# Kernel tuning notes

Hardware: AMD Instinct MI355X
Metric: run time of the kernel (lower is better)

## Reference

```python
import jax, jax.numpy as jnp
import numpy as np

M, Q, H, L = 1, 9, 512, 2

def lstm_seq(x, w_ih, w_hh, b, reverse=False):
    # x: [B, T, Din] -> outputs [B, T, H], final (h, c) each [B, H]
    B = x.shape[0]
    h0 = jnp.zeros((B, H), x.dtype)
    xw = jnp.einsum('btd,gd->btg', x, w_ih) + b  # [B, T, 4H] input projection, precomputed
    def step(carry, xt):
        h, c = carry
        g = xt + h @ w_hh.T
        i, f, gg, o = jnp.split(g, 4, axis=-1)  # torch gate order: i, f, g, o
        c = jax.nn.sigmoid(f) * c + jax.nn.sigmoid(i) * jnp.tanh(gg)
        h = jax.nn.sigmoid(o) * jnp.tanh(c)
        return (h, c), h
    (hT, cT), hs = jax.lax.scan(step, (h0, h0), jnp.swapaxes(xw, 0, 1), reverse=reverse)
    return jnp.swapaxes(hs, 0, 1), hT, cT

def _forward(X, future_features, Y_teacher,
             enc_w_ih_l0, enc_w_hh_l0, enc_b_l0, enc_w_ih_l0r, enc_w_hh_l0r, enc_b_l0r,
             enc_w_ih_l1, enc_w_hh_l1, enc_b_l1, enc_w_ih_l1r, enc_w_hh_l1r, enc_b_l1r,
             dec_w_ih_l0, dec_w_hh_l0, dec_b_l0, dec_w_ih_l1, dec_w_hh_l1, dec_b_l1,
             bidi_w_h, bidi_b_h, out_w, out_b, horizon_span):
    B = X.shape[0]
    enc = [((enc_w_ih_l0, enc_w_hh_l0, enc_b_l0), (enc_w_ih_l0r, enc_w_hh_l0r, enc_b_l0r)),
           ((enc_w_ih_l1, enc_w_hh_l1, enc_b_l1), (enc_w_ih_l1r, enc_w_hh_l1r, enc_b_l1r))]
    inp, hs, cs = X, [], []
    for fw, bw in enc:  # bidirectional multilayer encoder
        of, hf, cf = lstm_seq(inp, *fw, reverse=False)
        ob, hb, cb = lstm_seq(inp, *bw, reverse=True)
        inp = jnp.concatenate([of, ob], axis=-1)
        hs += [hf, hb]; cs += [cf, cb]
    h = jnp.stack(hs)  # [2L, B, H], torch order (l0_fwd, l0_bwd, l1_fwd, l1_bwd)
    c = jnp.stack(cs)
    def merge(s):  # NOTE: original applies bidi_project__h / nonlin__h to BOTH h and c
        s = s.reshape(L, 2, B, H)
        s = jnp.concatenate([s[:, 0], s[:, 1]], axis=2)       # [L, B, 2H]
        s = jnp.swapaxes(s, 0, 1).reshape(B, 2 * L * H)
        s = jax.nn.elu(s @ bidi_w_h.T + bidi_b_h)             # [B, L*H]
        return jnp.swapaxes(s.reshape(B, L, H), 0, 1)         # [L, B, H]
    h, c = merge(h), merge(c)
    dec = [(dec_w_ih_l0, dec_w_hh_l0, dec_b_l0), (dec_w_ih_l1, dec_w_hh_l1, dec_b_l1)]
    def dec_step(carry, f_t):
        h, c, y_prev = carry
        x = jnp.concatenate([y_prev, f_t], axis=-1)  # [B, M + d_future_features]
        nh, nc = [], []
        for l, (w_ih, w_hh, b) in enumerate(dec):
            g = x @ w_ih.T + h[l] @ w_hh.T + b
            i, f, gg, o = jnp.split(g, 4, axis=-1)
            cl = jax.nn.sigmoid(f) * c[l] + jax.nn.sigmoid(i) * jnp.tanh(gg)
            x = jax.nn.sigmoid(o) * jnp.tanh(cl)
            nh.append(x); nc.append(cl)
        y = x @ out_w.T + out_b                       # [B, M*Q]
        return (jnp.stack(nh), jnp.stack(nc), y[:, :M]), y
    y0 = X[:, -1, :M]
    _, ys = jax.lax.scan(dec_step, (h, c, y0), jnp.swapaxes(future_features, 0, 1))
    T = future_features.shape[1]
    return jnp.swapaxes(ys, 0, 1).reshape(B, T, M, Q)

def setup_inputs() -> dict:
    key = jax.random.key(0)
    ks = iter(jax.random.split(key, 40))
    s = 0.05
    d = {
        'X': jax.random.normal(next(ks), (64, 256, 9), jnp.float32),
        'future_features': jax.random.normal(next(ks), (64, 96, 8), jnp.float32),
        'Y_teacher': jax.random.normal(next(ks), (64, 96, 1), jnp.float32),
    }
    shapes = {
        'enc_w_ih_l0': (2048, 9), 'enc_w_hh_l0': (2048, 512), 'enc_b_l0': (2048,),
        'enc_w_ih_l0r': (2048, 9), 'enc_w_hh_l0r': (2048, 512), 'enc_b_l0r': (2048,),
        'enc_w_ih_l1': (2048, 1024), 'enc_w_hh_l1': (2048, 512), 'enc_b_l1': (2048,),
        'enc_w_ih_l1r': (2048, 1024), 'enc_w_hh_l1r': (2048, 512), 'enc_b_l1r': (2048,),
        'dec_w_ih_l0': (2048, 9), 'dec_w_hh_l0': (2048, 512), 'dec_b_l0': (2048,),
        'dec_w_ih_l1': (2048, 512), 'dec_w_hh_l1': (2048, 512), 'dec_b_l1': (2048,),
        'bidi_w_h': (1024, 2048), 'bidi_b_h': (1024,),
        'out_w': (9, 512), 'out_b': (9,),
    }
    for name, shp in shapes.items():
        d[name] = jax.random.normal(next(ks), shp, jnp.float32) * s
    d['horizon_span'] = 96
    return d

def reference(X, future_features, Y_teacher,
              enc_w_ih_l0, enc_w_hh_l0, enc_b_l0, enc_w_ih_l0r, enc_w_hh_l0r, enc_b_l0r,
              enc_w_ih_l1, enc_w_hh_l1, enc_b_l1, enc_w_ih_l1r, enc_w_hh_l1r, enc_b_l1r,
              dec_w_ih_l0, dec_w_hh_l0, dec_b_l0, dec_w_ih_l1, dec_w_hh_l1, dec_b_l1,
              bidi_w_h, bidi_b_h, out_w, out_b, horizon_span):
    return _forward(X, future_features, Y_teacher,
                    enc_w_ih_l0, enc_w_hh_l0, enc_b_l0, enc_w_ih_l0r, enc_w_hh_l0r, enc_b_l0r,
                    enc_w_ih_l1, enc_w_hh_l1, enc_b_l1, enc_w_ih_l1r, enc_w_hh_l1r, enc_b_l1r,
                    dec_w_ih_l0, dec_w_hh_l0, dec_b_l0, dec_w_ih_l1, dec_w_hh_l1, dec_b_l1,
                    bidi_w_h, bidi_b_h, out_w, out_b, horizon_span)
```

## Files before the change

### kernel.cpp

```cpp
#include <hip/hip_runtime.h>


#define BLOCKS 256

typedef short bf16x8 __attribute__((ext_vector_type(8)));
typedef float f32x4  __attribute__((ext_vector_type(4)));
typedef unsigned short u16;

__device__ __forceinline__ f32x4 MFMA16(bf16x8 a, bf16x8 b, f32x4 c) {
  return __builtin_amdgcn_mfma_f32_16x16x32_bf16(a, b, c, 0, 0, 0);
}

__device__ __forceinline__ u16 bfr(float f) {
  unsigned u = __float_as_uint(f);
  u += 0x7FFFu + ((u >> 16) & 1u);
  return (u16)(u >> 16);
}
__device__ __forceinline__ bf16x8 pack8(float4 a, float4 b) {
  bf16x8 r;
  r[0] = (short)bfr(a.x); r[1] = (short)bfr(a.y); r[2] = (short)bfr(a.z); r[3] = (short)bfr(a.w);
  r[4] = (short)bfr(b.x); r[5] = (short)bfr(b.y); r[6] = (short)bfr(b.z); r[7] = (short)bfr(b.w);
  return r;
}
__device__ __forceinline__ bf16x8 loadW8(const float* p) {
  float4 a = *(const float4*)p;
  float4 b = *(const float4*)(p + 4);
  return pack8(a, b);
}
__device__ __forceinline__ float sigm(float x) { return 1.0f / (1.0f + __expf(-x)); }
__device__ __forceinline__ float tanh_f(float x) {
  float a = fabsf(x);
  float e = __expf(-2.0f * a);
  float t = (1.0f - e) / (1.0f + e);
  return x < 0.0f ? -t : t;
}
__device__ __forceinline__ float lstm_h(const float pre[4], float& c) {
  float ig = sigm(pre[0]);
  float fg = sigm(pre[1]);
  float gg = tanh_f(pre[2]);
  float og = sigm(pre[3]);
  c = fg * c + ig * gg;
  return og * tanh_f(c);
}

__device__ __forceinline__ void st_b16_coh(u16* p, u16 v) {
  unsigned uv = v;
  asm volatile("global_store_short %0, %1, off sc0 sc1" :: "v"(p), "v"(uv) : "memory");
}
__device__ __forceinline__ void st_f32_coh(float* p, float v) {
  asm volatile("global_store_dword %0, %1, off sc0 sc1" :: "v"(p), "v"(v) : "memory");
}
__device__ __forceinline__ void st_u32_coh(unsigned* p, unsigned v) {
  asm volatile("global_store_dword %0, %1, off sc0 sc1" :: "v"(p), "v"(v) : "memory");
}
__device__ __forceinline__ float ld_f32_coh(const float* p) {
  float r;
  asm volatile("global_load_dword %0, %1, off sc0 sc1\n\ts_waitcnt vmcnt(0)"
               : "=&v"(r) : "v"(p) : "memory");
  return r;
}
__device__ __forceinline__ unsigned ld_u32_coh(const unsigned* p) {
  unsigned r;
  asm volatile("global_load_dword %0, %1, off sc0 sc1\n\ts_waitcnt vmcnt(0)"
               : "=&v"(r) : "v"(p) : "memory");
  return r;
}
__device__ __forceinline__ void ld_tile_coh(const u16* base, bf16x8 f[16]) {
  asm volatile(
    "global_load_dwordx4 %0, %16, off sc0 sc1\n\t"
    "global_load_dwordx4 %1, %16, off offset:64 sc0 sc1\n\t"
    "global_load_dwordx4 %2, %16, off offset:128 sc0 sc1\n\t"
    "global_load_dwordx4 %3, %16, off offset:192 sc0 sc1\n\t"
    "global_load_dwordx4 %4, %16, off offset:256 sc0 sc1\n\t"
    "global_load_dwordx4 %5, %16, off offset:320 sc0 sc1\n\t"
    "global_load_dwordx4 %6, %16, off offset:384 sc0 sc1\n\t"
    "global_load_dwordx4 %7, %16, off offset:448 sc0 sc1\n\t"
    "global_load_dwordx4 %8, %16, off offset:512 sc0 sc1\n\t"
    "global_load_dwordx4 %9, %16, off offset:576 sc0 sc1\n\t"
    "global_load_dwordx4 %10, %16, off offset:640 sc0 sc1\n\t"
    "global_load_dwordx4 %11, %16, off offset:704 sc0 sc1\n\t"
    "global_load_dwordx4 %12, %16, off offset:768 sc0 sc1\n\t"
    "global_load_dwordx4 %13, %16, off offset:832 sc0 sc1\n\t"
    "global_load_dwordx4 %14, %16, off offset:896 sc0 sc1\n\t"
    "global_load_dwordx4 %15, %16, off offset:960 sc0 sc1\n\t"
    "s_waitcnt vmcnt(0)"
    : "=&v"(f[0]), "=&v"(f[1]), "=&v"(f[2]), "=&v"(f[3]),
      "=&v"(f[4]), "=&v"(f[5]), "=&v"(f[6]), "=&v"(f[7]),
      "=&v"(f[8]), "=&v"(f[9]), "=&v"(f[10]), "=&v"(f[11]),
      "=&v"(f[12]), "=&v"(f[13]), "=&v"(f[14]), "=&v"(f[15])
    : "v"(base)
    : "memory");
}

static constexpr size_t OFF_GO   = 32768;
static constexpr size_t OFF_YF   = 32896;
static constexpr size_t SZ_SLOT  = (size_t)64 * 512 * 2;
static constexpr size_t OFF_OF   = 65536;
static constexpr size_t OFF_OBR  = OFF_OF  + 257 * SZ_SLOT;
static constexpr size_t OFF_H1F  = OFF_OBR + 257 * SZ_SLOT;
static constexpr size_t OFF_H1B  = OFF_H1F + 2 * SZ_SLOT;
static constexpr size_t OFF_DH0  = OFF_H1B + 2 * SZ_SLOT;
static constexpr size_t OFF_DH1  = OFF_DH0 + 2 * SZ_SLOT;
static constexpr size_t OFF_SBUF = OFF_DH1 + 2 * SZ_SLOT;
static constexpr size_t OFF_CDEC = OFF_SBUF + (size_t)128 * 2048 * 4;
static constexpr size_t OFF_Y    = OFF_CDEC + (size_t)2 * 64 * 512 * 4;
static constexpr size_t WS_NEED  = OFF_Y + 256;

__device__ __forceinline__ void gridbar(char* ws, unsigned e) {
  asm volatile("s_waitcnt vmcnt(0)" ::: "memory");
  __syncthreads();
  unsigned* flags = (unsigned*)ws;
  unsigned* go    = (unsigned*)(ws + OFF_GO);
  const int tid = threadIdx.x;
  if (blockIdx.x == 0) {
    if (tid != 0) {
      const unsigned* fp = flags + (size_t)tid * 32;
      while (ld_u32_coh(fp) < e) {}
    }
    __syncthreads();
    if (tid == 0) st_u32_coh(go, e);
  } else {
    if (tid == 0) {
      st_u32_coh(flags + (size_t)blockIdx.x * 32, e);
      while (ld_u32_coh(go) < e) { __builtin_amdgcn_s_sleep(1); }
    }
    __syncthreads();
  }
}

__global__ __launch_bounds__(256, 1) void red_lstm(
    const float* __restrict__ X,   const float* __restrict__ FUT,
    const float* __restrict__ eWih0,  const float* __restrict__ eWhh0,  const float* __restrict__ eB0,
    const float* __restrict__ eWih0r, const float* __restrict__ eWhh0r, const float* __restrict__ eB0r,
    const float* __restrict__ eWih1,  const float* __restrict__ eWhh1,  const float* __restrict__ eB1,
    const float* __restrict__ eWih1r, const float* __restrict__ eWhh1r, const float* __restrict__ eB1r,
    const float* __restrict__ dWih0,  const float* __restrict__ dWhh0,  const float* __restrict__ dB0,
    const float* __restrict__ dWih1,  const float* __restrict__ dWhh1,  const float* __restrict__ dB1,
    const float* __restrict__ bW,  const float* __restrict__ bB,
    const float* __restrict__ oW,  const float* __restrict__ oB,
    float* __restrict__ OUT, char* __restrict__ ws)
{
  const int blk  = blockIdx.x;
  const int tid  = threadIdx.x;
  const int lane = tid & 63;
  const int wave = tid >> 6;
  const int n16  = lane & 15;
  const int quad = lane >> 4;
  const int rowg = wave * 16 + n16;
  const int jl   = tid & 3;
  const int bb   = tid >> 2;

  u16*   OF  = (u16*)(ws + OFF_OF);
  u16*   OBR = (u16*)(ws + OFF_OBR);
  u16*   H1F = (u16*)(ws + OFF_H1F);
  u16*   H1B = (u16*)(ws + OFF_H1B);
  u16*   DH0 = (u16*)(ws + OFF_DH0);
  u16*   DH1 = (u16*)(ws + OFF_DH1);
  float* SB  = (float*)(ws + OFF_SBUF);
  float* CD  = (float*)(ws + OFF_CDEC);
  float* YB  = (float*)(ws + OFF_Y);
  unsigned* YFLAG = (unsigned*)(ws + OFF_YF);

  __shared__ float g_s[64 * 20];
  unsigned ep = 0;

  {
    const bool fw = (blk < 128);
    const int  hb = fw ? blk : (blk - 128);
    const int  j0 = hb * 4;
    const int  col = j0 + (n16 & 3) + 512 * (n16 >> 2);
    const float* whh = fw ? eWhh0 : eWhh0r;
    const float* wih = fw ? eWih0 : eWih0r;
    const float* bia = fw ? eB0 : eB0r;
    u16* buf = fw ? OF : OBR;

    bf16x8 B[16];
    {
      const float* wr = whh + (size_t)col * 512 + quad * 8;
      #pragma unroll
      for (int kk = 0; kk < 16; ++kk) B[kk] = loadW8(wr + kk * 32);
    }
    float wr9[4][9], b4[4];
    #pragma unroll
    for (int g = 0; g < 4; ++g) {
      int cg = j0 + jl + 512 * g;
      b4[g] = bia[cg];
      #pragma unroll
      for (int k = 0; k < 9; ++k) wr9[g][k] = wih[cg * 9 + k];
    }
    float c = 0.0f;

    #pragma unroll 1
    for (int s = 0; s < 256; ++s) {
      bf16x8 T[16];
      ld_tile_coh(buf + ((size_t)s * 64 + rowg) * 512 + quad * 8, T);
      f32x4 a0 = {0.f,0.f,0.f,0.f}, a1 = {0.f,0.f,0.f,0.f};
      #pragma unroll
      for (int kk = 0; kk < 16; kk += 2) {
        a0 = MFMA16(T[kk],     B[kk],     a0);
        a1 = MFMA16(T[kk + 1], B[kk + 1], a1);
      }
      f32x4 acc = a0 + a1;
      #pragma unroll
      for (int r = 0; r < 4; ++r)
        g_s[(wave * 16 + quad * 4 + r) * 20 + n16] = acc[r];
      __syncthreads();

      const int t = fw ? s : (255 - s);
      float pre[4];
      #pragma unroll
      for (int g = 0; g < 4; ++g) pre[g] = g_s[bb * 20 + jl + 4 * g] + b4[g];
      const float* xp = X + ((size_t)bb * 256 + t) * 9;
      #pragma unroll
      for (int k = 0; k < 9; ++k) {
        float xv = xp[k];
        #pragma unroll
        for (int g = 0; g < 4; ++g) pre[g] += xv * wr9[g][k];
      }
      float h = lstm_h(pre, c);
      st_b16_coh(buf + ((size_t)(s + 1) * 64 + bb) * 512 + j0 + jl, bfr(h));
      if (s == 255) {
        int co = fw ? 0 : 512;
        st_f32_coh(SB + (size_t)bb * 2048 + co + j0 + jl, h);
        st_f32_coh(SB + (size_t)(64 + bb) * 2048 + co + j0 + jl, c);
      }
      gridbar(ws, ++ep);
    }
  }

  {
    const bool fw = (blk < 128);
    const int  hb = fw ? blk : (blk - 128);
    const int  j0 = hb * 4;
    const int  col = j0 + (n16 & 3) + 512 * (n16 >> 2);
    const float* whh = fw ? eWhh1 : eWhh1r;
    const float* wih = fw ? eWih1 : eWih1r;
    const float* bia = fw ? eB1 : eB1r;
    u16* hpp = fw ? H1F : H1B;

    bf16x8 B[48];
    {
      const float* wr = whh + (size_t)col * 512 + quad * 8;
      #pragma unroll
      for (int kk = 0; kk < 16; ++kk) B[kk] = loadW8(wr + kk * 32);
      const float* wr2 = wih + (size_t)col * 1024 + quad * 8;
      #pragma unroll
      for (int kk = 0; kk < 32; ++kk) B[16 + kk] = loadW8(wr2 + kk * 32);
    }
    float b4[4];
    #pragma unroll
    for (int g = 0; g < 4; ++g) b4[g] = bia[j0 + jl + 512 * g];
    float c = 0.0f;

    #pragma unroll 1
    for (int s = 0; s < 256; ++s) {
      const int slot_of = fw ? (s + 1)   : (256 - s);
      const int slot_ob = fw ? (256 - s) : (s + 1);
      f32x4 a0 = {0.f,0.f,0.f,0.f}, a1 = {0.f,0.f,0.f,0.f};
      {
        bf16x8 T[16];
        ld_tile_coh(hpp + ((size_t)(s & 1) * 64 + rowg) * 512 + quad * 8, T);
        #pragma unroll
        for (int kk = 0; kk < 16; kk += 2) {
          a0 = MFMA16(T[kk],     B[kk],     a0);
          a1 = MFMA16(T[kk + 1], B[kk + 1], a1);
        }
      }
      {
        bf16x8 T[16];
        ld_tile_coh(OF + ((size_t)slot_of * 64 + rowg) * 512 + quad * 8, T);
        #pragma unroll
        for (int kk = 0; kk < 16; kk += 2) {
          a0 = MFMA16(T[kk],     B[16 + kk],     a0);
          a1 = MFMA16(T[kk + 1], B[16 + kk + 1], a1);
        }
      }
      {
        bf16x8 T[16];
        ld_tile_coh(OBR + ((size_t)slot_ob * 64 + rowg) * 512 + quad * 8, T);
        #pragma unroll
        for (int kk = 0; kk < 16; kk += 2) {
          a0 = MFMA16(T[kk],     B[32 + kk],     a0);
          a1 = MFMA16(T[kk + 1], B[32 + kk + 1], a1);
        }
      }
      f32x4 acc = a0 + a1;
      #pragma unroll
      for (int r = 0; r < 4; ++r)
        g_s[(wave * 16 + quad * 4 + r) * 20 + n16] = acc[r];
      __syncthreads();

      float pre[4];
      #pragma unroll
      for (int g = 0; g < 4; ++g) pre[g] = g_s[bb * 20 + jl + 4 * g] + b4[g];
      float h = lstm_h(pre, c);
      st_b16_coh(hpp + ((size_t)((s & 1) ^ 1) * 64 + bb) * 512 + j0 + jl, bfr(h));
      if (s == 255) {
        int co = fw ? 1024 : 1536;
        st_f32_coh(SB + (size_t)bb * 2048 + co + j0 + jl, h);
        st_f32_coh(SB + (size_t)(64 + bb) * 2048 + co + j0 + jl, c);
      }
      gridbar(ws, ++ep);
    }
  }

  {
    if (blk < 128) {
      const int colm = blk * 8 + (tid & 7);
      const int rg   = tid >> 3;
      const float* wrow = bW + (size_t)colm * 2048;
      float am[4];
      #pragma unroll
      for (int r = 0; r < 4; ++r) am[r] = bB[colm];
      #pragma unroll 1
      for (int k = 0; k < 2048; k += 4) {
        float4 w = *(const float4*)(wrow + k);
        #pragma unroll
        for (int r = 0; r < 4; ++r) {
          float4 a = *(const float4*)(SB + (size_t)(rg * 4 + r) * 2048 + k);
          am[r] += a.x * w.x + a.y * w.y + a.z * w.z + a.w * w.w;
        }
      }
      const int l = colm >> 9, j = colm & 511;
      #pragma unroll
      for (int r = 0; r < 4; ++r) {
        int row = rg * 4 + r;
        float v = am[r];
        v = v > 0.f ? v : (__expf(v) - 1.0f);
        if (row < 64) {
          u16* dst = l ? DH1 : DH0;
          st_b16_coh(dst + (size_t)row * 512 + j, bfr(v));
        } else {
          st_f32_coh(CD + ((size_t)l * 64 + (row - 64)) * 512 + j, v);
        }
      }
    }
    gridbar(ws, ++ep);
  }

  {
    const bool isL0 = (blk < 128);
    const int  hb = isL0 ? blk : (blk - 128);
    const int  j0 = hb * 4;
    const int  col = j0 + (n16 & 3) + 512 * (n16 >> 2);

    bf16x8 BD[32];
    float wr9[4][9], b4[4], c;
    if (isL0) {
      const float* wr = dWhh0 + (size_t)col * 512 + quad * 8;
      #pragma unroll
      for (int kk = 0; kk < 16; ++kk) BD[kk] = loadW8(wr + kk * 32);
      #pragma unroll
      for (int g = 0; g < 4; ++g) {
        int cg = j0 + jl + 512 * g;
        b4[g] = dB0[cg];
        #pragma unroll
        for (int k = 0; k < 9; ++k) wr9[g][k] = dWih0[cg * 9 + k];
      }
      c = CD[(size_t)bb * 512 + j0 + jl];
    } else {
      const float* wr = dWhh1 + (size_t)col * 512 + quad * 8;
      #pragma unroll
      for (int kk = 0; kk < 16; ++kk) BD[kk] = loadW8(wr + kk * 32);
      const float* wr2 = dWih1 + (size_t)col * 512 + quad * 8;
      #pragma unroll
      for (int kk = 0; kk < 16; ++kk) BD[16 + kk] = loadW8(wr2 + kk * 32);
      #pragma unroll
      for (int g = 0; g < 4; ++g) b4[g] = dB1[j0 + jl + 512 * g];
      c = CD[((size_t)64 + bb) * 512 + j0 + jl];
    }
    bf16x8 OBW[16];
    float obv = 0.0f;
    if (blk == 128) {
      if (n16 < 9) {
        const float* wr = oW + (size_t)n16 * 512 + quad * 8;
        #pragma unroll
        for (int kk = 0; kk < 16; ++kk) OBW[kk] = loadW8(wr + kk * 32);
        obv = oB[n16];
      } else {
        #pragma unroll
        for (int kk = 0; kk < 16; ++kk) {
          bf16x8 z = {0,0,0,0,0,0,0,0};
          OBW[kk] = z;
        }
      }
    }

    #pragma unroll 1
    for (int t = 0; t < 96; ++t) {
      if (blk == 128 && t >= 1) {
        bf16x8 T[16];
        ld_tile_coh(DH1 + ((size_t)(t & 1) * 64 + rowg) * 512 + quad * 8, T);
        f32x4 a0 = {0.f,0.f,0.f,0.f}, a1 = {0.f,0.f,0.f,0.f};
        #pragma unroll
        for (int kk = 0; kk < 16; kk += 2) {
          a0 = MFMA16(T[kk],     OBW[kk],     a0);
          a1 = MFMA16(T[kk + 1], OBW[kk + 1], a1);
        }
        f32x4 acc = a0 + a1;
        #pragma unroll
        for (int r = 0; r < 4; ++r) {
          int b = wave * 16 + quad * 4 + r;
          float v = acc[r] + obv;
          if (n16 < 9) {
            OUT[(size_t)b * 864 + (size_t)(t - 1) * 9 + n16] = v;
            if (n16 == 0) st_f32_coh(YB + b, v);
          }
        }
        asm volatile("s_waitcnt vmcnt(0)" ::: "memory");
        __syncthreads();
        if (tid == 0) st_u32_coh(YFLAG, (unsigned)t);
      }
      if (isL0) {
        bf16x8 T[16];
        ld_tile_coh(DH0 + ((size_t)(t & 1) * 64 + rowg) * 512 + quad * 8, T);
        f32x4 a0 = {0.f,0.f,0.f,0.f}, a1 = {0.f,0.f,0.f,0.f};
        #pragma unroll
        for (int kk = 0; kk < 16; kk += 2) {
          a0 = MFMA16(T[kk],     BD[kk],     a0);
          a1 = MFMA16(T[kk + 1], BD[kk + 1], a1);
        }
        f32x4 acc = a0 + a1;
        #pragma unroll
        for (int r = 0; r < 4; ++r)
          g_s[(wave * 16 + quad * 4 + r) * 20 + n16] = acc[r];
        __syncthreads();
        if (t >= 1 && tid == 0) {
          while (ld_u32_coh(YFLAG) < (unsigned)t) {}
        }
        __syncthreads();
        float pre[4];
        #pragma unroll
        for (int g = 0; g < 4; ++g) pre[g] = g_s[bb * 20 + jl + 4 * g] + b4[g];
        float yp = (t == 0) ? X[((size_t)bb * 256 + 255) * 9] : ld_f32_coh(YB + bb);
        #pragma unroll
        for (int g = 0; g < 4; ++g) pre[g] += yp * wr9[g][0];
        const float* fp = FUT + ((size_t)bb * 96 + t) * 8;
        #pragma unroll
        for (int k = 0; k < 8; ++k) {
          float fv = fp[k];
          #pragma unroll
          for (int g = 0; g < 4; ++g) pre[g] += fv * wr9[g][k + 1];
        }
        float h = lstm_h(pre, c);
        st_b16_coh(DH0 + ((size_t)((t & 1) ^ 1) * 64 + bb) * 512 + j0 + jl, bfr(h));
      }
      gridbar(ws, ++ep);

      if (!isL0) {
        f32x4 a0 = {0.f,0.f,0.f,0.f}, a1 = {0.f,0.f,0.f,0.f};
        {
          bf16x8 T[16];
          ld_tile_coh(DH1 + ((size_t)(t & 1) * 64 + rowg) * 512 + quad * 8, T);
          #pragma unroll
          for (int kk = 0; kk < 16; kk += 2) {
            a0 = MFMA16(T[kk],     BD[kk],     a0);
            a1 = MFMA16(T[kk + 1], BD[kk + 1], a1);
          }
        }
        {
          bf16x8 T[16];
          ld_tile_coh(DH0 + ((size_t)((t & 1) ^ 1) * 64 + rowg) * 512 + quad * 8, T);
          #pragma unroll
          for (int kk = 0; kk < 16; kk += 2) {
            a0 = MFMA16(T[kk],     BD[16 + kk],     a0);
            a1 = MFMA16(T[kk + 1], BD[16 + kk + 1], a1);
          }
        }
        f32x4 acc = a0 + a1;
        #pragma unroll
        for (int r = 0; r < 4; ++r)
          g_s[(wave * 16 + quad * 4 + r) * 20 + n16] = acc[r];
        __syncthreads();
        float pre[4];
        #pragma unroll
        for (int g = 0; g < 4; ++g) pre[g] = g_s[bb * 20 + jl + 4 * g] + b4[g];
        float h = lstm_h(pre, c);
        st_b16_coh(DH1 + ((size_t)((t & 1) ^ 1) * 64 + bb) * 512 + j0 + jl, bfr(h));
      }
      gridbar(ws, ++ep);
    }

    if (blk == 128) {
      bf16x8 T[16];
      ld_tile_coh(DH1 + ((size_t)0 * 64 + rowg) * 512 + quad * 8, T);
      f32x4 a0 = {0.f,0.f,0.f,0.f}, a1 = {0.f,0.f,0.f,0.f};
      #pragma unroll
      for (int kk = 0; kk < 16; kk += 2) {
        a0 = MFMA16(T[kk],     OBW[kk],     a0);
        a1 = MFMA16(T[kk + 1], OBW[kk + 1], a1);
      }
      f32x4 acc = a0 + a1;
      #pragma unroll
      for (int r = 0; r < 4; ++r) {
        int b = wave * 16 + quad * 4 + r;
        float v = acc[r] + obv;
        if (n16 < 9) OUT[(size_t)b * 864 + (size_t)95 * 9 + n16] = v;
      }
    }
  }
}

extern "C" void kernel_launch(void* const* d_in, const int* in_sizes, int n_in,
                              void* d_out, int out_size, void* d_ws, size_t ws_size,
                              hipStream_t stream) {
  (void)in_sizes; (void)n_in; (void)out_size;
  if (ws_size < WS_NEED) return;

  const float* X      = (const float*)d_in[0];
  const float* FUT    = (const float*)d_in[1];
  const float* eWih0  = (const float*)d_in[3];
  const float* eWhh0  = (const float*)d_in[4];
  const float* eB0    = (const float*)d_in[5];
  const float* eWih0r = (const float*)d_in[6];
  const float* eWhh0r = (const float*)d_in[7];
  const float* eB0r   = (const float*)d_in[8];
  const float* eWih1  = (const float*)d_in[9];
  const float* eWhh1  = (const float*)d_in[10];
  const float* eB1    = (const float*)d_in[11];
  const float* eWih1r = (const float*)d_in[12];
  const float* eWhh1r = (const float*)d_in[13];
  const float* eB1r   = (const float*)d_in[14];
  const float* dWih0  = (const float*)d_in[15];
  const float* dWhh0  = (const float*)d_in[16];
  const float* dB0    = (const float*)d_in[17];
  const float* dWih1  = (const float*)d_in[18];
  const float* dWhh1  = (const float*)d_in[19];
  const float* dB1    = (const float*)d_in[20];
  const float* bW     = (const float*)d_in[21];
  const float* bB     = (const float*)d_in[22];
  const float* oW     = (const float*)d_in[23];
  const float* oB     = (const float*)d_in[24];

  char* ws = (char*)d_ws;
  hipMemsetAsync(ws, 0, 65536, stream);
  hipMemsetAsync(ws + OFF_OF, 0, SZ_SLOT, stream);
  hipMemsetAsync(ws + OFF_OBR, 0, SZ_SLOT, stream);
  hipMemsetAsync(ws + OFF_H1F, 0, SZ_SLOT, stream);
  hipMemsetAsync(ws + OFF_H1B, 0, SZ_SLOT, stream);

  red_lstm<<<BLOCKS, 256, 0, stream>>>(
      X, FUT,
      eWih0, eWhh0, eB0, eWih0r, eWhh0r, eB0r,
      eWih1, eWhh1, eB1, eWih1r, eWhh1r, eB1r,
      dWih0, dWhh0, dB0, dWih1, dWhh1, dB1,
      bW, bB, oW, oB,
      (float*)d_out, ws);
}
```

Before: 4.603 ms.

## Replace per-step grid barriers with sentinel-polled dataflow synchronization

Removes the global grid barrier after every encoder and decoder timestep. Each timestep's hidden state now gets its own slot, pre-filled with 0xFF sentinels by memsets, and consumers poll the tiles they need until no sentinel word remains. The decoder output projection is folded into the layer-0 blocks, which removes the separate y flag handshake, and hidden states are stored as packed pairs. The cost is much larger workspace memsets on every call, extra polling traffic, and reliance on a bf16 value never matching the all-ones pattern.

```diff
diff --git a/kernel.cpp b/kernel.cpp
--- a/kernel.cpp
+++ b/kernel.cpp
@@ -5,6 +5,7 @@
 
 typedef short bf16x8 __attribute__((ext_vector_type(8)));
 typedef float f32x4  __attribute__((ext_vector_type(4)));
+typedef unsigned u32x4 __attribute__((ext_vector_type(4)));
 typedef unsigned short u16;
 
 __device__ __forceinline__ f32x4 MFMA16(bf16x8 a, bf16x8 b, f32x4 c) {
@@ -42,15 +43,12 @@
   c = fg * c + ig * gg;
   return og * tanh_f(c);
 }
-
-__device__ __forceinline__ void st_b16_coh(u16* p, u16 v) {
-  unsigned uv = v;
-  asm volatile("global_store_short %0, %1, off sc0 sc1" :: "v"(p), "v"(uv) : "memory");
+__device__ __forceinline__ float elu(float v) { return v > 0.f ? v : (__expf(v) - 1.0f); }
+
+__device__ __forceinline__ void st_u32_coh(unsigned* p, unsigned v) {
+  asm volatile("global_store_dword %0, %1, off sc0 sc1" :: "v"(p), "v"(v) : "memory");
 }
 __device__ __forceinline__ void st_f32_coh(float* p, float v) {
-  asm volatile("global_store_dword %0, %1, off sc0 sc1" :: "v"(p), "v"(v) : "memory");
-}
-__device__ __forceinline__ void st_u32_coh(unsigned* p, unsigned v) {
   asm volatile("global_store_dword %0, %1, off sc0 sc1" :: "v"(p), "v"(v) : "memory");
 }
 __device__ __forceinline__ float ld_f32_coh(const float* p) {
@@ -59,9 +57,9 @@
                : "=&v"(r) : "v"(p) : "memory");
   return r;
 }
-__device__ __forceinline__ unsigned ld_u32_coh(const unsigned* p) {
-  unsigned r;
-  asm volatile("global_load_dword %0, %1, off sc0 sc1\n\ts_waitcnt vmcnt(0)"
+__device__ __forceinline__ u32x4 ld_u32x4_coh(const unsigned* p) {
+  u32x4 r;
+  asm volatile("global_load_dwordx4 %0, %1, off sc0 sc1\n\ts_waitcnt vmcnt(0)"
                : "=&v"(r) : "v"(p) : "memory");
   return r;
 }
@@ -91,41 +89,107 @@
     : "v"(base)
     : "memory");
 }
-
-static constexpr size_t OFF_GO   = 32768;
-static constexpr size_t OFF_YF   = 32896;
+__device__ __forceinline__ void ld_tile_issue(const u16* base, bf16x8 f[16]) {
+  asm volatile(
+    "global_load_dwordx4 %0, %16, off sc0 sc1\n\t"
+    "global_load_dwordx4 %1, %16, off offset:64 sc0 sc1\n\t"
+    "global_load_dwordx4 %2, %16, off offset:128 sc0 sc1\n\t"
+    "global_load_dwordx4 %3, %16, off offset:192 sc0 sc1\n\t"
+    "global_load_dwordx4 %4, %16, off offset:256 sc0 sc1\n\t"
+    "global_load_dwordx4 %5, %16, off offset:320 sc0 sc1\n\t"
+    "global_load_dwordx4 %6, %16, off offset:384 sc0 sc1\n\t"
+    "global_load_dwordx4 %7, %16, off offset:448 sc0 sc1\n\t"
+    "global_load_dwordx4 %8, %16, off offset:512 sc0 sc1\n\t"
+    "global_load_dwordx4 %9, %16, off offset:576 sc0 sc1\n\t"
+    "global_load_dwordx4 %10, %16, off offset:640 sc0 sc1\n\t"
+    "global_load_dwordx4 %11, %16, off offset:704 sc0 sc1\n\t"
+    "global_load_dwordx4 %12, %16, off offset:768 sc0 sc1\n\t"
+    "global_load_dwordx4 %13, %16, off offset:832 sc0 sc1\n\t"
+    "global_load_dwordx4 %14, %16, off offset:896 sc0 sc1\n\t"
+    "global_load_dwordx4 %15, %16, off offset:960 sc0 sc1"
+    : "=&v"(f[0]), "=&v"(f[1]), "=&v"(f[2]), "=&v"(f[3]),
+      "=&v"(f[4]), "=&v"(f[5]), "=&v"(f[6]), "=&v"(f[7]),
+      "=&v"(f[8]), "=&v"(f[9]), "=&v"(f[10]), "=&v"(f[11]),
+      "=&v"(f[12]), "=&v"(f[13]), "=&v"(f[14]), "=&v"(f[15])
+    : "v"(base)
+    : "memory");
+}
+
+__device__ __forceinline__ unsigned tile_max(const bf16x8 f[16]) {
+  unsigned m = 0u;
+  #pragma unroll
+  for (int k = 0; k < 16; ++k) {
+    u32x4 w = __builtin_bit_cast(u32x4, f[k]);
+    unsigned a = w.x > w.y ? w.x : w.y;
+    unsigned b = w.z > w.w ? w.z : w.w;
+    unsigned cm = a > b ? a : b;
+    m = m > cm ? m : cm;
+  }
+  return m;
+}
+__device__ __forceinline__ void poll_tile(const u16* base, bf16x8 f[16]) {
+  ld_tile_coh(base, f);
+  int miss = 0;
+  while (__any(tile_max(f) == 0xFFFFFFFFu)) {
+    if (++miss > 2) __builtin_amdgcn_s_sleep(2);
+    ld_tile_coh(base, f);
+  }
+}
+__device__ __forceinline__ void poll_tile2(const u16* b0, const u16* b1,
+                                           bf16x8 f0[16], bf16x8 f1[16]) {
+  ld_tile_issue(b0, f0);
+  ld_tile_issue(b1, f1);
+  asm volatile("s_waitcnt vmcnt(0)" ::: "memory");
+  __builtin_amdgcn_sched_barrier(0);
+  int miss = 0;
+  while (__any(tile_max(f0) == 0xFFFFFFFFu)) {
+    if (++miss > 2) __builtin_amdgcn_s_sleep(2);
+    ld_tile_coh(b0, f0);
+  }
+  miss = 0;
+  while (__any(tile_max(f1) == 0xFFFFFFFFu)) {
+    if (++miss > 2) __builtin_amdgcn_s_sleep(2);
+    ld_tile_coh(b1, f1);
+  }
+}
+__device__ __forceinline__ float poll_f32(const float* p) {
+  float v = ld_f32_coh(p);
+  int miss = 0;
+  while (__float_as_uint(v) == 0xFFFFFFFFu) {
+    if (++miss > 2) __builtin_amdgcn_s_sleep(2);
+    v = ld_f32_coh(p);
+  }
+  return v;
+}
+
 static constexpr size_t SZ_SLOT  = (size_t)64 * 512 * 2;
 static constexpr size_t OFF_OF   = 65536;
 static constexpr size_t OFF_OBR  = OFF_OF  + 257 * SZ_SLOT;
 static constexpr size_t OFF_H1F  = OFF_OBR + 257 * SZ_SLOT;
-static constexpr size_t OFF_H1B  = OFF_H1F + 2 * SZ_SLOT;
-static constexpr size_t OFF_DH0  = OFF_H1B + 2 * SZ_SLOT;
-static constexpr size_t OFF_DH1  = OFF_DH0 + 2 * SZ_SLOT;
-static constexpr size_t OFF_SBUF = OFF_DH1 + 2 * SZ_SLOT;
+static constexpr size_t OFF_H1B  = OFF_H1F + 257 * SZ_SLOT;
+static constexpr size_t OFF_DH0  = OFF_H1B + 257 * SZ_SLOT;
+static constexpr size_t OFF_DH1  = OFF_DH0 + 97 * SZ_SLOT;
+static constexpr size_t OFF_SBUF = OFF_DH1 + 97 * SZ_SLOT;
 static constexpr size_t OFF_CDEC = OFF_SBUF + (size_t)128 * 2048 * 4;
-static constexpr size_t OFF_Y    = OFF_CDEC + (size_t)2 * 64 * 512 * 4;
-static constexpr size_t WS_NEED  = OFF_Y + 256;
-
-__device__ __forceinline__ void gridbar(char* ws, unsigned e) {
+static constexpr size_t WS_NEED  = OFF_CDEC + (size_t)2 * 64 * 512 * 4;
+
+__device__ __forceinline__ void gridbar1(char* ws) {
   asm volatile("s_waitcnt vmcnt(0)" ::: "memory");
   __syncthreads();
   unsigned* flags = (unsigned*)ws;
-  unsigned* go    = (unsigned*)(ws + OFF_GO);
-  const int tid = threadIdx.x;
-  if (blockIdx.x == 0) {
-    if (tid != 0) {
-      const unsigned* fp = flags + (size_t)tid * 32;
-      while (ld_u32_coh(fp) < e) {}
-    }
-    __syncthreads();
-    if (tid == 0) st_u32_coh(go, e);
-  } else {
-    if (tid == 0) {
-      st_u32_coh(flags + (size_t)blockIdx.x * 32, e);
-      while (ld_u32_coh(go) < e) { __builtin_amdgcn_s_sleep(1); }
-    }
-    __syncthreads();
-  }
+  if (threadIdx.x == 0) st_u32_coh(flags + blockIdx.x, 1u);
+  if (threadIdx.x < 64) {
+    int miss = 0;
+    for (;;) {
+      u32x4 f4 = ld_u32x4_coh(flags + (size_t)threadIdx.x * 4);
+      unsigned a = f4.x < f4.y ? f4.x : f4.y;
+      unsigned b = f4.z < f4.w ? f4.z : f4.w;
+      unsigned mn = a < b ? a : b;
+      if (!__any(mn == 0u)) break;
+      if (++miss > 4) __builtin_amdgcn_s_sleep(2);
+    }
+  }
+  __syncthreads();
 }
 
 __global__ __launch_bounds__(256, 1) void red_lstm(
@@ -158,11 +222,8 @@
   u16*   DH1 = (u16*)(ws + OFF_DH1);
   float* SB  = (float*)(ws + OFF_SBUF);
   float* CD  = (float*)(ws + OFF_CDEC);
-  float* YB  = (float*)(ws + OFF_Y);
-  unsigned* YFLAG = (unsigned*)(ws + OFF_YF);
 
   __shared__ float g_s[64 * 20];
-  unsigned ep = 0;
 
   {
     const bool fw = (blk < 128);
@@ -193,7 +254,7 @@
     #pragma unroll 1
     for (int s = 0; s < 256; ++s) {
       bf16x8 T[16];
-      ld_tile_coh(buf + ((size_t)s * 64 + rowg) * 512 + quad * 8, T);
+      poll_tile(buf + ((size_t)s * 64 + rowg) * 512 + quad * 8, T);
       f32x4 a0 = {0.f,0.f,0.f,0.f}, a1 = {0.f,0.f,0.f,0.f};
       #pragma unroll
       for (int kk = 0; kk < 16; kk += 2) {
@@ -218,13 +279,17 @@
         for (int g = 0; g < 4; ++g) pre[g] += xv * wr9[g][k];
       }
       float h = lstm_h(pre, c);
-      st_b16_coh(buf + ((size_t)(s + 1) * 64 + bb) * 512 + j0 + jl, bfr(h));
+      float hn = __shfl_down(h, 1);
+      if ((jl & 1) == 0) {
+        unsigned pk = (unsigned)bfr(h) | ((unsigned)bfr(hn) << 16);
+        st_u32_coh((unsigned*)(buf + ((size_t)(s + 1) * 64 + bb) * 512 + j0 + jl), pk);
+      }
       if (s == 255) {
         int co = fw ? 0 : 512;
         st_f32_coh(SB + (size_t)bb * 2048 + co + j0 + jl, h);
         st_f32_coh(SB + (size_t)(64 + bb) * 2048 + co + j0 + jl, c);
       }
-      gridbar(ws, ++ep);
+      __syncthreads();
     }
   }
 
@@ -236,7 +301,7 @@
     const float* whh = fw ? eWhh1 : eWhh1r;
     const float* wih = fw ? eWih1 : eWih1r;
     const float* bia = fw ? eB1 : eB1r;
-    u16* hpp = fw ? H1F : H1B;
+    u16* hsl = fw ? H1F : H1B;
 
     bf16x8 B[48];
     {
@@ -256,34 +321,49 @@
     for (int s = 0; s < 256; ++s) {
       const int slot_of = fw ? (s + 1)   : (256 - s);
       const int slot_ob = fw ? (256 - s) : (s + 1);
+      const u16* pof = OF  + ((size_t)slot_of * 64 + rowg) * 512 + quad * 8;
+      const u16* pob = OBR + ((size_t)slot_ob * 64 + rowg) * 512 + quad * 8;
       f32x4 a0 = {0.f,0.f,0.f,0.f}, a1 = {0.f,0.f,0.f,0.f};
+      if (s == 0) {
+        bf16x8 T[16];
+        poll_tile(pof, T);
+        #pragma unroll
+        for (int kk = 0; kk < 16; kk += 2) {
+          a0 = MFMA16(T[kk],     B[16 + kk],     a0);
+          a1 = MFMA16(T[kk + 1], B[16 + kk + 1], a1);
+        }
+        poll_tile(pob, T);
+        #pragma unroll
+        for (int kk = 0; kk < 16; kk += 2) {
+          a0 = MFMA16(T[kk],     B[32 + kk],     a0);
+          a1 = MFMA16(T[kk + 1], B[32 + kk + 1], a1);
+        }
+      } else {
+        bf16x8 T[16];
+        #pragma unroll
+        for (int kk = 0; kk < 16; ++kk) T[kk] = *(const bf16x8*)(pof + kk * 32);
+        #pragma unroll
+        for (int kk = 0; kk < 16; kk += 2) {
+          a0 = MFMA16(T[kk],     B[16 + kk],     a0);
+          a1 = MFMA16(T[kk + 1], B[16 + kk + 1], a1);
+        }
+        #pragma unroll
+        for (int kk = 0; kk < 16; ++kk) T[kk] = *(const bf16x8*)(pob + kk * 32);
+        #pragma unroll
+        for (int kk = 0; kk < 16; kk += 2) {
+          a0 = MFMA16(T[kk],     B[32 + kk],     a0);
+          a1 = MFMA16(T[kk + 1], B[32 + kk + 1], a1);
+        }
+      }
       {
         bf16x8 T[16];
-        ld_tile_coh(hpp + ((size_t)(s & 1) * 64 + rowg) * 512 + quad * 8, T);
+        poll_tile(hsl + ((size_t)s * 64 + rowg) * 512 + quad * 8, T);
         #pragma unroll
         for (int kk = 0; kk < 16; kk += 2) {
           a0 = MFMA16(T[kk],     B[kk],     a0);
           a1 = MFMA16(T[kk + 1], B[kk + 1], a1);
         }
       }
-      {
-        bf16x8 T[16];
-        ld_tile_coh(OF + ((size_t)slot_of * 64 + rowg) * 512 + quad * 8, T);
-        #pragma unroll
-        for (int kk = 0; kk < 16; kk += 2) {
-          a0 = MFMA16(T[kk],     B[16 + kk],     a0);
-          a1 = MFMA16(T[kk + 1], B[16 + kk + 1], a1);
-        }
-      }
-      {
-        bf16x8 T[16];
-        ld_tile_coh(OBR + ((size_t)slot_ob * 64 + rowg) * 512 + quad * 8, T);
-        #pragma unroll
-        for (int kk = 0; kk < 16; kk += 2) {
-          a0 = MFMA16(T[kk],     B[32 + kk],     a0);
-          a1 = MFMA16(T[kk + 1], B[32 + kk + 1], a1);
-        }
-      }
       f32x4 acc = a0 + a1;
       #pragma unroll
       for (int r = 0; r < 4; ++r)
@@ -294,81 +374,157 @@
       #pragma unroll
       for (int g = 0; g < 4; ++g) pre[g] = g_s[bb * 20 + jl + 4 * g] + b4[g];
       float h = lstm_h(pre, c);
-      st_b16_coh(hpp + ((size_t)((s & 1) ^ 1) * 64 + bb) * 512 + j0 + jl, bfr(h));
+      float hn = __shfl_down(h, 1);
+      if ((jl & 1) == 0) {
+        unsigned pk = (unsigned)bfr(h) | ((unsigned)bfr(hn) << 16);
+        st_u32_coh((unsigned*)(hsl + ((size_t)(s + 1) * 64 + bb) * 512 + j0 + jl), pk);
+      }
       if (s == 255) {
         int co = fw ? 1024 : 1536;
         st_f32_coh(SB + (size_t)bb * 2048 + co + j0 + jl, h);
         st_f32_coh(SB + (size_t)(64 + bb) * 2048 + co + j0 + jl, c);
       }
-      gridbar(ws, ++ep);
-    }
-  }
-
-  {
-    if (blk < 128) {
-      const int colm = blk * 8 + (tid & 7);
-      const int rg   = tid >> 3;
-      const float* wrow = bW + (size_t)colm * 2048;
-      float am[4];
-      #pragma unroll
-      for (int r = 0; r < 4; ++r) am[r] = bB[colm];
-      #pragma unroll 1
-      for (int k = 0; k < 2048; k += 4) {
-        float4 w = *(const float4*)(wrow + k);
-        #pragma unroll
-        for (int r = 0; r < 4; ++r) {
-          float4 a = *(const float4*)(SB + (size_t)(rg * 4 + r) * 2048 + k);
-          am[r] += a.x * w.x + a.y * w.y + a.z * w.z + a.w * w.w;
-        }
-      }
-      const int l = colm >> 9, j = colm & 511;
+      __syncthreads();
+    }
+  }
+
+  gridbar1(ws);
+
+  if (blk < 128 && tid < 128) {
+    const int cp = tid & 3;
+    const int rg = tid >> 2;
+    const int c0 = blk * 8 + cp * 2;
+    const float* w0 = bW + (size_t)c0 * 2048;
+    const float* w1 = w0 + 2048;
+    float am0[4], am1[4];
+    #pragma unroll
+    for (int r = 0; r < 4; ++r) { am0[r] = bB[c0]; am1[r] = bB[c0 + 1]; }
+    #pragma unroll 1
+    for (int k = 0; k < 2048; k += 4) {
+      float4 wa = *(const float4*)(w0 + k);
+      float4 wb = *(const float4*)(w1 + k);
       #pragma unroll
       for (int r = 0; r < 4; ++r) {
-        int row = rg * 4 + r;
-        float v = am[r];
-        v = v > 0.f ? v : (__expf(v) - 1.0f);
-        if (row < 64) {
-          u16* dst = l ? DH1 : DH0;
-          st_b16_coh(dst + (size_t)row * 512 + j, bfr(v));
-        } else {
-          st_f32_coh(CD + ((size_t)l * 64 + (row - 64)) * 512 + j, v);
-        }
-      }
-    }
-    gridbar(ws, ++ep);
-  }
-
-  {
-    const bool isL0 = (blk < 128);
-    const int  hb = isL0 ? blk : (blk - 128);
-    const int  j0 = hb * 4;
-    const int  col = j0 + (n16 & 3) + 512 * (n16 >> 2);
-
+        float4 a = *(const float4*)(SB + (size_t)(rg * 4 + r) * 2048 + k);
+        am0[r] += a.x * wa.x + a.y * wa.y + a.z * wa.z + a.w * wa.w;
+        am1[r] += a.x * wb.x + a.y * wb.y + a.z * wb.z + a.w * wb.w;
+      }
+    }
+    const int l = c0 >> 9, j = c0 & 511;
+    #pragma unroll
+    for (int r = 0; r < 4; ++r) {
+      int row = rg * 4 + r;
+      float v0 = elu(am0[r]);
+      float v1 = elu(am1[r]);
+      if (row < 64) {
+        u16* dst = l ? DH1 : DH0;
+        unsigned pk = (unsigned)bfr(v0) | ((unsigned)bfr(v1) << 16);
+        st_u32_coh((unsigned*)(dst + (size_t)row * 512 + j), pk);
+      } else {
+        st_f32_coh(CD + ((size_t)l * 64 + (row - 64)) * 512 + j, v0);
+        st_f32_coh(CD + ((size_t)l * 64 + (row - 64)) * 512 + j + 1, v1);
+      }
+    }
+  }
+
+  if (blk < 128) {
+    const int j0 = blk * 4;
+    const int col = j0 + (n16 & 3) + 512 * (n16 >> 2);
+    bf16x8 BD[16], OW0[16];
+    {
+      const float* wr = dWhh0 + (size_t)col * 512 + quad * 8;
+      #pragma unroll
+      for (int kk = 0; kk < 16; ++kk) BD[kk] = loadW8(wr + kk * 32);
+    }
+    #pragma unroll
+    for (int kk = 0; kk < 16; ++kk) {
+      if (n16 == 0) OW0[kk] = loadW8(oW + quad * 8 + kk * 32);
+      else { bf16x8 z = {0,0,0,0,0,0,0,0}; OW0[kk] = z; }
+    }
+    float wr9[4][9], b4[4];
+    #pragma unroll
+    for (int g = 0; g < 4; ++g) {
+      int cg = j0 + jl + 512 * g;
+      b4[g] = dB0[cg];
+      #pragma unroll
+      for (int k = 0; k < 9; ++k) wr9[g][k] = dWih0[cg * 9 + k];
+    }
+    const float ob0 = oB[0];
+    float c = poll_f32(CD + (size_t)bb * 512 + j0 + jl);
+    const float xlast = X[((size_t)bb * 256 + 255) * 9];
+
+    #pragma unroll 1
+    for (int t = 0; t < 96; ++t) {
+      bf16x8 T0[16], T1[16];
+      const u16* p0 = DH0 + ((size_t)t * 64 + rowg) * 512 + quad * 8;
+      if (t == 0) {
+        poll_tile(p0, T0);
+      } else {
+        poll_tile2(p0, DH1 + ((size_t)t * 64 + rowg) * 512 + quad * 8, T0, T1);
+      }
+      f32x4 a0 = {0.f,0.f,0.f,0.f}, a1 = {0.f,0.f,0.f,0.f};
+      #pragma unroll
+      for (int kk = 0; kk < 16; kk += 2) {
+        a0 = MFMA16(T0[kk],     BD[kk],     a0);
+        a1 = MFMA16(T0[kk + 1], BD[kk + 1], a1);
+      }
+      f32x4 acc = a0 + a1;
+      #pragma unroll
+      for (int r = 0; r < 4; ++r)
+        g_s[(wave * 16 + quad * 4 + r) * 20 + n16] = acc[r];
+      if (t >= 1) {
+        f32x4 y0 = {0.f,0.f,0.f,0.f}, y1 = {0.f,0.f,0.f,0.f};
+        #pragma unroll
+        for (int kk = 0; kk < 16; kk += 2) {
+          y0 = MFMA16(T1[kk],     OW0[kk],     y0);
+          y1 = MFMA16(T1[kk + 1], OW0[kk + 1], y1);
+        }
+        f32x4 accy = y0 + y1;
+        if (n16 == 0) {
+          #pragma unroll
+          for (int r = 0; r < 4; ++r)
+            g_s[(wave * 16 + quad * 4 + r) * 20 + 16] = accy[r] + ob0;
+        }
+      }
+      __syncthreads();
+
+      float pre[4];
+      #pragma unroll
+      for (int g = 0; g < 4; ++g) pre[g] = g_s[bb * 20 + jl + 4 * g] + b4[g];
+      float yp = (t == 0) ? xlast : g_s[bb * 20 + 16];
+      #pragma unroll
+      for (int g = 0; g < 4; ++g) pre[g] += yp * wr9[g][0];
+      const float* fp = FUT + ((size_t)bb * 96 + t) * 8;
+      #pragma unroll
+      for (int k = 0; k < 8; ++k) {
+        float fv = fp[k];
+        #pragma unroll
+        for (int g = 0; g < 4; ++g) pre[g] += fv * wr9[g][k + 1];
+      }
+      float h = lstm_h(pre, c);
+      float hn = __shfl_down(h, 1);
+      if ((jl & 1) == 0) {
+        unsigned pk = (unsigned)bfr(h) | ((unsigned)bfr(hn) << 16);
+        st_u32_coh((unsigned*)(DH0 + ((size_t)(t + 1) * 64 + bb) * 512 + j0 + jl), pk);
+      }
+      __syncthreads();
+    }
+  } else {
+    const int hb = blk - 128;
+    const int j0 = hb * 4;
+    const int col = j0 + (n16 & 3) + 512 * (n16 >> 2);
     bf16x8 BD[32];
-    float wr9[4][9], b4[4], c;
-    if (isL0) {
-      const float* wr = dWhh0 + (size_t)col * 512 + quad * 8;
-      #pragma unroll
-      for (int kk = 0; kk < 16; ++kk) BD[kk] = loadW8(wr + kk * 32);
-      #pragma unroll
-      for (int g = 0; g < 4; ++g) {
-        int cg = j0 + jl + 512 * g;
-        b4[g] = dB0[cg];
-        #pragma unroll
-        for (int k = 0; k < 9; ++k) wr9[g][k] = dWih0[cg * 9 + k];
-      }
-      c = CD[(size_t)bb * 512 + j0 + jl];
-    } else {
+    {
       const float* wr = dWhh1 + (size_t)col * 512 + quad * 8;
       #pragma unroll
       for (int kk = 0; kk < 16; ++kk) BD[kk] = loadW8(wr + kk * 32);
       const float* wr2 = dWih1 + (size_t)col * 512 + quad * 8;
       #pragma unroll
       for (int kk = 0; kk < 16; ++kk) BD[16 + kk] = loadW8(wr2 + kk * 32);
-      #pragma unroll
-      for (int g = 0; g < 4; ++g) b4[g] = dB1[j0 + jl + 512 * g];
-      c = CD[((size_t)64 + bb) * 512 + j0 + jl];
-    }
+    }
+    float b4[4];
+    #pragma unroll
+    for (int g = 0; g < 4; ++g) b4[g] = dB1[j0 + jl + 512 * g];
     bf16x8 OBW[16];
     float obv = 0.0f;
     if (blk == 128) {
@@ -379,122 +535,73 @@
         obv = oB[n16];
       } else {
         #pragma unroll
-        for (int kk = 0; kk < 16; ++kk) {
-          bf16x8 z = {0,0,0,0,0,0,0,0};
-          OBW[kk] = z;
-        }
-      }
-    }
+        for (int kk = 0; kk < 16; ++kk) { bf16x8 z = {0,0,0,0,0,0,0,0}; OBW[kk] = z; }
+      }
+    }
+    float c = poll_f32(CD + ((size_t)64 + bb) * 512 + j0 + jl);
 
     #pragma unroll 1
     for (int t = 0; t < 96; ++t) {
+      bf16x8 Th1[16], T0[16];
+      poll_tile2(DH1 + ((size_t)t * 64 + rowg) * 512 + quad * 8,
+                 DH0 + ((size_t)(t + 1) * 64 + rowg) * 512 + quad * 8, Th1, T0);
+      f32x4 a0 = {0.f,0.f,0.f,0.f}, a1 = {0.f,0.f,0.f,0.f};
+      #pragma unroll
+      for (int kk = 0; kk < 16; kk += 2) {
+        a0 = MFMA16(Th1[kk],     BD[kk],     a0);
+        a1 = MFMA16(Th1[kk + 1], BD[kk + 1], a1);
+      }
+      #pragma unroll
+      for (int kk = 0; kk < 16; kk += 2) {
+        a0 = MFMA16(T0[kk],     BD[16 + kk],     a0);
+        a1 = MFMA16(T0[kk + 1], BD[16 + kk + 1], a1);
+      }
+      f32x4 acc = a0 + a1;
+      #pragma unroll
+      for (int r = 0; r < 4; ++r)
+        g_s[(wave * 16 + quad * 4 + r) * 20 + n16] = acc[r];
+      __syncthreads();
+
+      float pre[4];
+      #pragma unroll
+      for (int g = 0; g < 4; ++g) pre[g] = g_s[bb * 20 + jl + 4 * g] + b4[g];
+      float h = lstm_h(pre, c);
+      float hn = __shfl_down(h, 1);
+      if ((jl & 1) == 0) {
+        unsigned pk = (unsigned)bfr(h) | ((unsigned)bfr(hn) << 16);
+        st_u32_coh((unsigned*)(DH1 + ((size_t)(t + 1) * 64 + bb) * 512 + j0 + jl), pk);
+      }
       if (blk == 128 && t >= 1) {
-        bf16x8 T[16];
-        ld_tile_coh(DH1 + ((size_t)(t & 1) * 64 + rowg) * 512 + quad * 8, T);
-        f32x4 a0 = {0.f,0.f,0.f,0.f}, a1 = {0.f,0.f,0.f,0.f};
+        f32x4 y0 = {0.f,0.f,0.f,0.f}, y1 = {0.f,0.f,0.f,0.f};
         #pragma unroll
         for (int kk = 0; kk < 16; kk += 2) {
-          a0 = MFMA16(T[kk],     OBW[kk],     a0);
-          a1 = MFMA16(T[kk + 1], OBW[kk + 1], a1);
-        }
-        f32x4 acc = a0 + a1;
+          y0 = MFMA16(Th1[kk],     OBW[kk],     y0);
+          y1 = MFMA16(Th1[kk + 1], OBW[kk + 1], y1);
+        }
+        f32x4 accy = y0 + y1;
         #pragma unroll
         for (int r = 0; r < 4; ++r) {
           int b = wave * 16 + quad * 4 + r;
-          float v = acc[r] + obv;
-          if (n16 < 9) {
-            OUT[(size_t)b * 864 + (size_t)(t - 1) * 9 + n16] = v;
-            if (n16 == 0) st_f32_coh(YB + b, v);
-          }
-        }
-        asm volatile("s_waitcnt vmcnt(0)" ::: "memory");
-        __syncthreads();
-        if (tid == 0) st_u32_coh(YFLAG, (unsigned)t);
-      }
-      if (isL0) {
-        bf16x8 T[16];
-        ld_tile_coh(DH0 + ((size_t)(t & 1) * 64 + rowg) * 512 + quad * 8, T);
-        f32x4 a0 = {0.f,0.f,0.f,0.f}, a1 = {0.f,0.f,0.f,0.f};
-        #pragma unroll
-        for (int kk = 0; kk < 16; kk += 2) {
-          a0 = MFMA16(T[kk],     BD[kk],     a0);
-          a1 = MFMA16(T[kk + 1], BD[kk + 1], a1);
-        }
-        f32x4 acc = a0 + a1;
-        #pragma unroll
-        for (int r = 0; r < 4; ++r)
-          g_s[(wave * 16 + quad * 4 + r) * 20 + n16] = acc[r];
-        __syncthreads();
-        if (t >= 1 && tid == 0) {
-          while (ld_u32_coh(YFLAG) < (unsigned)t) {}
-        }
-        __syncthreads();
-        float pre[4];
-        #pragma unroll
-        for (int g = 0; g < 4; ++g) pre[g] = g_s[bb * 20 + jl + 4 * g] + b4[g];
-        float yp = (t == 0) ? X[((size_t)bb * 256 + 255) * 9] : ld_f32_coh(YB + bb);
-        #pragma unroll
-        for (int g = 0; g < 4; ++g) pre[g] += yp * wr9[g][0];
-        const float* fp = FUT + ((size_t)bb * 96 + t) * 8;
-        #pragma unroll
-        for (int k = 0; k < 8; ++k) {
-          float fv = fp[k];
-          #pragma unroll
-          for (int g = 0; g < 4; ++g) pre[g] += fv * wr9[g][k + 1];
-        }
-        float h = lstm_h(pre, c);
-        st_b16_coh(DH0 + ((size_t)((t & 1) ^ 1) * 64 + bb) * 512 + j0 + jl, bfr(h));
-      }
-      gridbar(ws, ++ep);
-
-      if (!isL0) {
-        f32x4 a0 = {0.f,0.f,0.f,0.f}, a1 = {0.f,0.f,0.f,0.f};
-        {
-          bf16x8 T[16];
-          ld_tile_coh(DH1 + ((size_t)(t & 1) * 64 + rowg) * 512 + quad * 8, T);
-          #pragma unroll
-          for (int kk = 0; kk < 16; kk += 2) {
-            a0 = MFMA16(T[kk],     BD[kk],     a0);
-            a1 = MFMA16(T[kk + 1], BD[kk + 1], a1);
-          }
-        }
-        {
-          bf16x8 T[16];
-          ld_tile_coh(DH0 + ((size_t)((t & 1) ^ 1) * 64 + rowg) * 512 + quad * 8, T);
-          #pragma unroll
-          for (int kk = 0; kk < 16; kk += 2) {
-            a0 = MFMA16(T[kk],     BD[16 + kk],     a0);
-            a1 = MFMA16(T[kk + 1], BD[16 + kk + 1], a1);
-          }
-        }
-        f32x4 acc = a0 + a1;
-        #pragma unroll
-        for (int r = 0; r < 4; ++r)
-          g_s[(wave * 16 + quad * 4 + r) * 20 + n16] = acc[r];
-        __syncthreads();
-        float pre[4];
-        #pragma unroll
-        for (int g = 0; g < 4; ++g) pre[g] = g_s[bb * 20 + jl + 4 * g] + b4[g];
-        float h = lstm_h(pre, c);
-        st_b16_coh(DH1 + ((size_t)((t & 1) ^ 1) * 64 + bb) * 512 + j0 + jl, bfr(h));
-      }
-      gridbar(ws, ++ep);
-    }
-
+          float v = accy[r] + obv;
+          if (n16 < 9) OUT[(size_t)b * 864 + (size_t)(t - 1) * 9 + n16] = v;
+        }
+      }
+      __syncthreads();
+    }
     if (blk == 128) {
       bf16x8 T[16];
-      ld_tile_coh(DH1 + ((size_t)0 * 64 + rowg) * 512 + quad * 8, T);
-      f32x4 a0 = {0.f,0.f,0.f,0.f}, a1 = {0.f,0.f,0.f,0.f};
+      poll_tile(DH1 + ((size_t)96 * 64 + rowg) * 512 + quad * 8, T);
+      f32x4 y0 = {0.f,0.f,0.f,0.f}, y1 = {0.f,0.f,0.f,0.f};
       #pragma unroll
       for (int kk = 0; kk < 16; kk += 2) {
-        a0 = MFMA16(T[kk],     OBW[kk],     a0);
-        a1 = MFMA16(T[kk + 1], OBW[kk + 1], a1);
-      }
-      f32x4 acc = a0 + a1;
+        y0 = MFMA16(T[kk],     OBW[kk],     y0);
+        y1 = MFMA16(T[kk + 1], OBW[kk + 1], y1);
+      }
+      f32x4 accy = y0 + y1;
       #pragma unroll
       for (int r = 0; r < 4; ++r) {
         int b = wave * 16 + quad * 4 + r;
-        float v = acc[r] + obv;
+        float v = accy[r] + obv;
         if (n16 < 9) OUT[(size_t)b * 864 + (size_t)95 * 9 + n16] = v;
       }
     }
@@ -533,11 +640,18 @@
   const float* oB     = (const float*)d_in[24];
 
   char* ws = (char*)d_ws;
-  hipMemsetAsync(ws, 0, 65536, stream);
-  hipMemsetAsync(ws + OFF_OF, 0, SZ_SLOT, stream);
-  hipMemsetAsync(ws + OFF_OBR, 0, SZ_SLOT, stream);
-  hipMemsetAsync(ws + OFF_H1F, 0, SZ_SLOT, stream);
-  hipMemsetAsync(ws + OFF_H1B, 0, SZ_SLOT, stream);
+  hipMemsetAsync(ws, 0, 4096, stream);
+  hipMemsetAsync(ws + OFF_OF,            0x00, SZ_SLOT, stream);
+  hipMemsetAsync(ws + OFF_OF + SZ_SLOT,  0xFF, 256 * SZ_SLOT, stream);
+  hipMemsetAsync(ws + OFF_OBR,           0x00, SZ_SLOT, stream);
+  hipMemsetAsync(ws + OFF_OBR + SZ_SLOT, 0xFF, 256 * SZ_SLOT, stream);
+  hipMemsetAsync(ws + OFF_H1F,           0x00, SZ_SLOT, stream);
+  hipMemsetAsync(ws + OFF_H1F + SZ_SLOT, 0xFF, 256 * SZ_SLOT, stream);
+  hipMemsetAsync(ws + OFF_H1B,           0x00, SZ_SLOT, stream);
+  hipMemsetAsync(ws + OFF_H1B + SZ_SLOT, 0xFF, 256 * SZ_SLOT, stream);
+  hipMemsetAsync(ws + OFF_DH0,           0xFF, 97 * SZ_SLOT, stream);
+  hipMemsetAsync(ws + OFF_DH1,           0xFF, 97 * SZ_SLOT, stream);
+  hipMemsetAsync(ws + OFF_CDEC,          0xFF, (size_t)2 * 64 * 512 * 4, stream);
 
   red_lstm<<<BLOCKS, 256, 0, stream>>>(
       X, FUT,
```

Result: slower. 5.702 ms (+23.9%).
